# Kernel optimization log

Hardware: AMD Instinct MI355X
Metric: run time of the kernel (lower is better)

The kernel has to match this reference:

```python
import jax, jax.numpy as jnp
import numpy as np

NORMALIZE_EPS = 1e-5
INV_DELTA = 15.0
DIST_NORM_PREV = 0.5  # init value of _dist_norm_prev buffer (eval-mode constant)
SKIP_OFFSET = 2


def _l2_normalize(v, axis, eps=NORMALIZE_EPS):
    # matches torch F.normalize: v / max(||v||, eps)
    n = jnp.sqrt(jnp.sum(v * v, axis=axis, keepdims=True))
    return v / jnp.maximum(n, eps)


def setup_inputs() -> dict:
    key = jax.random.key(0)
    k1, k2 = jax.random.split(key)
    x = jax.random.normal(k1, (128, 197, 768), dtype=jnp.float32)
    emb = jnp.clip(jax.random.normal(k2, (4096, 768), dtype=jnp.float32), 0.0, None)
    emb = _l2_normalize(emb, axis=1)
    return {"x": x, "embedding": emb}


def reference(x, embedding):
    # drop CLS token -> [N, L, C] with L = H*W
    x = x[:, 1:, :]
    N, L, C = x.shape
    height = width = int(np.sqrt(L))
    # assign_words: L2-normalize tokens, cosine distance to codebook
    xn = _l2_normalize(x, axis=2)
    dist = -jnp.einsum("nlc,kc->nlk", xn, embedding)  # [N, L, K]
    inv_delta = INV_DELTA / DIST_NORM_PREV
    codes = jax.nn.softmax(-inv_delta * dist, axis=2)  # [N, L, K]
    # compute_bow: drop border tokens, mean-pool, L1-normalize
    grid = jnp.arange(height * width).reshape(height, width)
    keep = grid[SKIP_OFFSET:-SKIP_OFFSET, SKIP_OFFSET:-SKIP_OFFSET].reshape(-1)
    bow = jnp.mean(codes[:, keep, :], axis=1)  # [N, K]
    bow = bow / jnp.maximum(jnp.sum(jnp.abs(bow), axis=1, keepdims=True), NORMALIZE_EPS)
    return bow, codes
```

## Files before the change

kernel.cpp:

```cpp
#include <hip/hip_runtime.h>


typedef unsigned short ushort_t;
typedef short short8 __attribute__((ext_vector_type(8)));
typedef float float4_ __attribute__((ext_vector_type(4)));

#define M_ROWS 25088
#define N_COLS 4096
#define K_DIM  768
#define BM 128
#define BN 128
#define BK 32
#define K_STEPS (K_DIM / BK)

__device__ __forceinline__ unsigned short f2bf_rne(float f) {
  unsigned u = __float_as_uint(f);
  unsigned r = u + 0x7fffu + ((u >> 16) & 1u);
  return (unsigned short)(r >> 16);
}
__device__ __forceinline__ float bf2f(unsigned short h) {
  return __uint_as_float(((unsigned)h) << 16);
}

__device__ __forceinline__ void gload16(const void* g, void* l) {
  __builtin_amdgcn_global_load_lds(
      (__attribute__((address_space(1))) void*)g,
      (__attribute__((address_space(3))) void*)l, 16, 0, 0);
}

__global__ void split_emb_kernel(const float* __restrict__ emb,
                                 ushort_t* __restrict__ Bh,
                                 ushort_t* __restrict__ Bl) {
  int t = blockIdx.x * 256 + threadIdx.x;
  float f = emb[t];
  unsigned short h = f2bf_rne(f);
  Bh[t] = h;
  Bl[t] = f2bf_rne(f - bf2f(h));
}

__global__ void norm_split_x_kernel(const float* __restrict__ x,
                                    ushort_t* __restrict__ Ah,
                                    ushort_t* __restrict__ Al) {
  int m = blockIdx.x;
  int n = m / 196;
  int l = m - n * 196;
  size_t src = ((size_t)n * 197 + 1 + l) * 768;
  int t = threadIdx.x;

  float v0 = x[src + t];
  float v1 = x[src + t + 256];
  float v2 = x[src + t + 512];
  float s = v0 * v0 + v1 * v1 + v2 * v2;
  #pragma unroll
  for (int off = 32; off; off >>= 1) s += __shfl_xor(s, off, 64);
  __shared__ float ws4[4];
  if ((t & 63) == 0) ws4[t >> 6] = s;
  __syncthreads();
  s = ws4[0] + ws4[1] + ws4[2] + ws4[3];
  float scale = 1.0f / fmaxf(sqrtf(s), 1e-5f);

  size_t dst = (size_t)m * 768;
  float f[3] = {v0 * scale, v1 * scale, v2 * scale};
  int idx[3] = {t, t + 256, t + 512};
  #pragma unroll
  for (int i = 0; i < 3; i++) {
    unsigned short h = f2bf_rne(f[i]);
    Ah[dst + idx[i]] = h;
    Al[dst + idx[i]] = f2bf_rne(f[i] - bf2f(h));
  }
}

__global__ __launch_bounds__(256, 2)
void gemm_exp_kernel(const ushort_t* __restrict__ Ah, const ushort_t* __restrict__ Al,
                     const ushort_t* __restrict__ Bh, const ushort_t* __restrict__ Bl,
                     float* __restrict__ codes, float* __restrict__ rowsum) {
  __shared__ __attribute__((aligned(16))) ushort_t sAh[2][BM * BK];
  __shared__ __attribute__((aligned(16))) ushort_t sAl[2][BM * BK];
  __shared__ __attribute__((aligned(16))) ushort_t sBh[2][BM * BK];
  __shared__ __attribute__((aligned(16))) ushort_t sBl[2][BM * BK];
  __shared__ float rs[BM];

  const int t = threadIdx.x;
  const int w = t >> 6;
  const int lane = t & 63;
  const int row0 = blockIdx.x * BM;
  const int col0 = blockIdx.y * BN;

  if (t < BM) rs[t] = 0.f;

  float4_ acc[4][4];
  #pragma unroll
  for (int i = 0; i < 4; i++)
    #pragma unroll
    for (int j = 0; j < 4; j++) acc[i][j] = (float4_){0.f, 0.f, 0.f, 0.f};

  const int r0 = t >> 2;
  const int c0 = (((t & 3) ^ ((r0 >> 1) & 3))) * 8;
  const ushort_t* gA = Ah + (size_t)(row0 + r0) * K_DIM + c0;
  const ushort_t* gAl_ = Al + (size_t)(row0 + r0) * K_DIM + c0;
  const ushort_t* gB = Bh + (size_t)(col0 + r0) * K_DIM + c0;
  const ushort_t* gBl_ = Bl + (size_t)(col0 + r0) * K_DIM + c0;
  const int half = 64 * K_DIM;
  const int ldsw = w * 512;

  const int rl = (w >> 1) * 64;
  const int cl = (w & 1) * 64;
  const int lq = lane >> 4;
  const int li = lane & 15;
  const int fsw = (li >> 1) & 3;
  const int abase = (rl + li) * BK + (lq ^ fsw) * 8;
  const int bbase = (cl + li) * BK + (lq ^ fsw) * 8;

  auto issue = [&](int b, int kk) {
    gload16(gA + kk,           &sAh[b][ldsw]);
    gload16(gA + kk + half,    &sAh[b][2048 + ldsw]);
    gload16(gAl_ + kk,         &sAl[b][ldsw]);
    gload16(gAl_ + kk + half,  &sAl[b][2048 + ldsw]);
    gload16(gB + kk,           &sBh[b][ldsw]);
    gload16(gB + kk + half,    &sBh[b][2048 + ldsw]);
    gload16(gBl_ + kk,         &sBl[b][ldsw]);
    gload16(gBl_ + kk + half,  &sBl[b][2048 + ldsw]);
  };

  auto compute = [&](int b) {
    short8 ah[4], al[4], bh[4], bl[4];
    #pragma unroll
    for (int i = 0; i < 4; i++) {
      ah[i] = *(const short8*)(&sAh[b][abase + i * 16 * BK]);
      al[i] = *(const short8*)(&sAl[b][abase + i * 16 * BK]);
      bh[i] = *(const short8*)(&sBh[b][bbase + i * 16 * BK]);
      bl[i] = *(const short8*)(&sBl[b][bbase + i * 16 * BK]);
    }
    #pragma unroll
    for (int i = 0; i < 4; i++)
      #pragma unroll
      for (int j = 0; j < 4; j++) {
        acc[i][j] = __builtin_amdgcn_mfma_f32_16x16x32_bf16(ah[i], bh[j], acc[i][j], 0, 0, 0);
        acc[i][j] = __builtin_amdgcn_mfma_f32_16x16x32_bf16(ah[i], bl[j], acc[i][j], 0, 0, 0);
        acc[i][j] = __builtin_amdgcn_mfma_f32_16x16x32_bf16(al[i], bh[j], acc[i][j], 0, 0, 0);
      }
  };

  issue(0, 0);

  #pragma unroll 1
  for (int ks = 0; ks < K_STEPS - 2; ks += 2) {
    issue(1, (ks + 1) * BK);
    asm volatile("s_waitcnt vmcnt(8)" ::: "memory");
    __builtin_amdgcn_s_barrier();
    asm volatile("" ::: "memory");
    compute(0);
    asm volatile("" ::: "memory");
    __builtin_amdgcn_s_barrier();

    issue(0, (ks + 2) * BK);
    asm volatile("s_waitcnt vmcnt(8)" ::: "memory");
    __builtin_amdgcn_s_barrier();
    asm volatile("" ::: "memory");
    compute(1);
    asm volatile("" ::: "memory");
    __builtin_amdgcn_s_barrier();
  }

  issue(1, (K_STEPS - 1) * BK);
  asm volatile("s_waitcnt vmcnt(8)" ::: "memory");
  __builtin_amdgcn_s_barrier();
  asm volatile("" ::: "memory");
  compute(0);
  asm volatile("" ::: "memory");
  __builtin_amdgcn_s_barrier();

  asm volatile("s_waitcnt vmcnt(0)" ::: "memory");
  __builtin_amdgcn_s_barrier();
  asm volatile("" ::: "memory");
  compute(1);

  float rsum[4][4];
  #pragma unroll
  for (int i = 0; i < 4; i++)
    #pragma unroll
    for (int r = 0; r < 4; r++) rsum[i][r] = 0.f;

  #pragma unroll
  for (int i = 0; i < 4; i++)
    #pragma unroll
    for (int j = 0; j < 4; j++)
      #pragma unroll
      for (int r = 0; r < 4; r++) {
        float e = __expf(30.0f * acc[i][j][r]);
        size_t row = (size_t)(row0 + rl + i * 16 + lq * 4 + r);
        size_t col = (size_t)(col0 + cl + j * 16 + li);
        codes[row * N_COLS + col] = e;
        rsum[i][r] += e;
      }

  #pragma unroll
  for (int i = 0; i < 4; i++)
    #pragma unroll
    for (int r = 0; r < 4; r++) {
      float v = rsum[i][r];
      v += __shfl_xor(v, 1, 64);
      v += __shfl_xor(v, 2, 64);
      v += __shfl_xor(v, 4, 64);
      v += __shfl_xor(v, 8, 64);
      if (li == 0) atomicAdd(&rs[rl + i * 16 + lq * 4 + r], v);
    }
  __syncthreads();
  if (t < BM) atomicAdd(&rowsum[row0 + t], rs[t]);
}

__global__ __launch_bounds__(256)
void rescale_bow_kernel(float* __restrict__ codes,
                        const float* __restrict__ rowsum,
                        float* __restrict__ bow_un) {
  const int bid = blockIdx.x;
  const int n = bid >> 4;
  const int g = (bid >> 2) & 3;
  const int chunk = bid & 3;
  const int t = threadIdx.x;
  const int k4 = chunk * 256 + t;
  const int l0 = g * 49;

  __shared__ float inv[49];
  __shared__ float keep[49];
  if (t < 49) {
    int l = l0 + t;
    inv[t] = 1.0f / rowsum[n * 196 + l];
    int rr = l / 14;
    int cc = l - rr * 14;
    keep[t] = (rr >= 2 && rr <= 11 && cc >= 2 && cc <= 11) ? 0.01f : 0.0f;
  }
  __syncthreads();

  float4_* base = (float4_*)(codes + (size_t)n * 196 * N_COLS)
                  + (size_t)l0 * 1024 + k4;
  float4_ acc = {0.f, 0.f, 0.f, 0.f};
  #pragma unroll
  for (int c = 0; c < 7; c++) {
    float4_ v[7];
    #pragma unroll
    for (int u = 0; u < 7; u++) v[u] = base[(size_t)(c * 7 + u) * 1024];
    #pragma unroll
    for (int u = 0; u < 7; u++) {
      int l = c * 7 + u;
      float iv = inv[l];
      v[u].x *= iv; v[u].y *= iv; v[u].z *= iv; v[u].w *= iv;
      base[(size_t)l * 1024] = v[u];
      float kf = keep[l];
      acc.x += kf * v[u].x; acc.y += kf * v[u].y;
      acc.z += kf * v[u].z; acc.w += kf * v[u].w;
    }
  }

  float* dst = bow_un + (size_t)n * N_COLS + (size_t)k4 * 4;
  atomicAdd(dst + 0, acc.x);
  atomicAdd(dst + 1, acc.y);
  atomicAdd(dst + 2, acc.z);
  atomicAdd(dst + 3, acc.w);
}

__global__ __launch_bounds__(256)
void bow_norm_kernel(const float* __restrict__ bow_un,
                     float* __restrict__ bow_out) {
  const int n = blockIdx.x;
  const int t = threadIdx.x;
  const float4_* src = (const float4_*)(bow_un + (size_t)n * N_COLS);
  float4_ v[4];
  float s = 0.f;
  #pragma unroll
  for (int i = 0; i < 4; i++) {
    v[i] = src[t + i * 256];
    s += fabsf(v[i].x) + fabsf(v[i].y) + fabsf(v[i].z) + fabsf(v[i].w);
  }
  #pragma unroll
  for (int off = 32; off; off >>= 1) s += __shfl_xor(s, off, 64);
  __shared__ float ws4[4];
  if ((t & 63) == 0) ws4[t >> 6] = s;
  __syncthreads();
  float invn = 1.0f / fmaxf(ws4[0] + ws4[1] + ws4[2] + ws4[3], 1e-5f);
  float4_* dst = (float4_*)(bow_out + (size_t)n * N_COLS);
  #pragma unroll
  for (int i = 0; i < 4; i++) {
    float4_ o = v[i];
    o.x *= invn; o.y *= invn; o.z *= invn; o.w *= invn;
    dst[t + i * 256] = o;
  }
}

extern "C" void kernel_launch(void* const* d_in, const int* in_sizes, int n_in,
                              void* d_out, int out_size, void* d_ws, size_t ws_size,
                              hipStream_t stream) {
  const float* x = (const float*)d_in[0];
  const float* emb = (const float*)d_in[1];
  float* bow_out = (float*)d_out;
  float* codes = (float*)d_out + 524288;

  char* ws = (char*)d_ws;
  ushort_t* Ah = (ushort_t*)(ws + 0);
  ushort_t* Al = (ushort_t*)(ws + 38535168);
  ushort_t* Bh = (ushort_t*)(ws + 77070336);
  ushort_t* Bl = (ushort_t*)(ws + 83361792);
  float* rowsum = (float*)(ws + 89653248);
  float* bow_un = (float*)(ws + 89753600);

  hipMemsetAsync(rowsum, 0, 25088 * 4, stream);
  hipMemsetAsync(bow_un, 0, 524288 * 4, stream);

  split_emb_kernel<<<12288, 256, 0, stream>>>(emb, Bh, Bl);
  norm_split_x_kernel<<<25088, 256, 0, stream>>>(x, Ah, Al);

  dim3 ggrid(M_ROWS / BM, N_COLS / BN);
  gemm_exp_kernel<<<ggrid, 256, 0, stream>>>(Ah, Al, Bh, Bl, codes, rowsum);

  rescale_bow_kernel<<<2048, 256, 0, stream>>>(codes, rowsum, bow_un);
  bow_norm_kernel<<<128, 256, 0, stream>>>(bow_un, bow_out);
}
```

Baseline: 1.057 ms.

## Swap GEMM grid order and restructure rescale/bow reduction without atomics

Swaps the GEMM grid so consecutive blocks walk across codebook columns for the same row tile, which changes L2 reuse of the A rows versus the B panel. Each rescale block now processes all 196 tokens for its column chunk, so bow_un is written directly instead of via per-element atomics and its memset goes away. The L1 norm is accumulated per sample with one atomic per block, and the final normalize becomes a simple elementwise kernel. The rescale grid shrinks from 2048 to 512 blocks, which lowers parallelism for that memory-bound pass.

New measurement: 1.018 ms. -3.7%, faster.

```diff
diff --git a/kernel.cpp b/kernel.cpp
--- a/kernel.cpp
+++ b/kernel.cpp
@@ -83,8 +83,8 @@
   const int t = threadIdx.x;
   const int w = t >> 6;
   const int lane = t & 63;
-  const int row0 = blockIdx.x * BM;
-  const int col0 = blockIdx.y * BN;
+  const int row0 = blockIdx.y * BM;
+  const int col0 = blockIdx.x * BN;
 
   if (t < BM) rs[t] = 0.f;
 
@@ -212,37 +212,32 @@
 __global__ __launch_bounds__(256)
 void rescale_bow_kernel(float* __restrict__ codes,
                         const float* __restrict__ rowsum,
-                        float* __restrict__ bow_un) {
-  const int bid = blockIdx.x;
-  const int n = bid >> 4;
-  const int g = (bid >> 2) & 3;
-  const int chunk = bid & 3;
+                        float* __restrict__ bow_un,
+                        float* __restrict__ bow_l1) {
+  const int n = blockIdx.x >> 2;
   const int t = threadIdx.x;
-  const int k4 = chunk * 256 + t;
-  const int l0 = g * 49;
-
-  __shared__ float inv[49];
-  __shared__ float keep[49];
-  if (t < 49) {
-    int l = l0 + t;
-    inv[t] = 1.0f / rowsum[n * 196 + l];
-    int rr = l / 14;
-    int cc = l - rr * 14;
+  const int k4 = (blockIdx.x & 3) * 256 + t;
+
+  __shared__ float inv[196];
+  __shared__ float keep[196];
+  if (t < 196) {
+    inv[t] = 1.0f / rowsum[n * 196 + t];
+    int rr = t / 14;
+    int cc = t - rr * 14;
     keep[t] = (rr >= 2 && rr <= 11 && cc >= 2 && cc <= 11) ? 0.01f : 0.0f;
   }
   __syncthreads();
 
-  float4_* base = (float4_*)(codes + (size_t)n * 196 * N_COLS)
-                  + (size_t)l0 * 1024 + k4;
+  float4_* base = (float4_*)(codes + (size_t)n * 196 * N_COLS) + k4;
   float4_ acc = {0.f, 0.f, 0.f, 0.f};
-  #pragma unroll
-  for (int c = 0; c < 7; c++) {
-    float4_ v[7];
-    #pragma unroll
-    for (int u = 0; u < 7; u++) v[u] = base[(size_t)(c * 7 + u) * 1024];
-    #pragma unroll
-    for (int u = 0; u < 7; u++) {
-      int l = c * 7 + u;
+  #pragma unroll 1
+  for (int c = 0; c < 14; c++) {
+    float4_ v[14];
+    #pragma unroll
+    for (int u = 0; u < 14; u++) v[u] = base[(size_t)(c * 14 + u) * 1024];
+    #pragma unroll
+    for (int u = 0; u < 14; u++) {
+      int l = c * 14 + u;
       float iv = inv[l];
       v[u].x *= iv; v[u].y *= iv; v[u].z *= iv; v[u].w *= iv;
       base[(size_t)l * 1024] = v[u];
@@ -252,39 +247,23 @@
     }
   }
 
-  float* dst = bow_un + (size_t)n * N_COLS + (size_t)k4 * 4;
-  atomicAdd(dst + 0, acc.x);
-  atomicAdd(dst + 1, acc.y);
-  atomicAdd(dst + 2, acc.z);
-  atomicAdd(dst + 3, acc.w);
-}
-
-__global__ __launch_bounds__(256)
-void bow_norm_kernel(const float* __restrict__ bow_un,
-                     float* __restrict__ bow_out) {
-  const int n = blockIdx.x;
-  const int t = threadIdx.x;
-  const float4_* src = (const float4_*)(bow_un + (size_t)n * N_COLS);
-  float4_ v[4];
-  float s = 0.f;
-  #pragma unroll
-  for (int i = 0; i < 4; i++) {
-    v[i] = src[t + i * 256];
-    s += fabsf(v[i].x) + fabsf(v[i].y) + fabsf(v[i].z) + fabsf(v[i].w);
-  }
+  ((float4_*)(bow_un + (size_t)n * N_COLS))[k4] = acc;
+
+  float s = fabsf(acc.x) + fabsf(acc.y) + fabsf(acc.z) + fabsf(acc.w);
   #pragma unroll
   for (int off = 32; off; off >>= 1) s += __shfl_xor(s, off, 64);
-  __shared__ float ws4[4];
-  if ((t & 63) == 0) ws4[t >> 6] = s;
-  __syncthreads();
-  float invn = 1.0f / fmaxf(ws4[0] + ws4[1] + ws4[2] + ws4[3], 1e-5f);
-  float4_* dst = (float4_*)(bow_out + (size_t)n * N_COLS);
-  #pragma unroll
-  for (int i = 0; i < 4; i++) {
-    float4_ o = v[i];
-    o.x *= invn; o.y *= invn; o.z *= invn; o.w *= invn;
-    dst[t + i * 256] = o;
-  }
+  __shared__ float wsum[4];
+  if ((t & 63) == 0) wsum[t >> 6] = s;
+  __syncthreads();
+  if (t == 0) atomicAdd(&bow_l1[n], wsum[0] + wsum[1] + wsum[2] + wsum[3]);
+}
+
+__global__ void bow_norm_kernel(const float* __restrict__ bow_un,
+                                const float* __restrict__ bow_l1,
+                                float* __restrict__ bow_out) {
+  int t = blockIdx.x * 256 + threadIdx.x;
+  int n = t >> 12;
+  bow_out[t] = bow_un[t] / fmaxf(bow_l1[n], 1e-5f);
 }
 
 extern "C" void kernel_launch(void* const* d_in, const int* in_sizes, int n_in,
@@ -302,16 +281,17 @@
   ushort_t* Bl = (ushort_t*)(ws + 83361792);
   float* rowsum = (float*)(ws + 89653248);
   float* bow_un = (float*)(ws + 89753600);
+  float* bow_l1 = (float*)(ws + 91850752);
 
   hipMemsetAsync(rowsum, 0, 25088 * 4, stream);
-  hipMemsetAsync(bow_un, 0, 524288 * 4, stream);
+  hipMemsetAsync(bow_l1, 0, 128 * 4, stream);
 
   split_emb_kernel<<<12288, 256, 0, stream>>>(emb, Bh, Bl);
   norm_split_x_kernel<<<25088, 256, 0, stream>>>(x, Ah, Al);
 
-  dim3 ggrid(M_ROWS / BM, N_COLS / BN);
+  dim3 ggrid(N_COLS / BN, M_ROWS / BM);
   gemm_exp_kernel<<<ggrid, 256, 0, stream>>>(Ah, Al, Bh, Bl, codes, rowsum);
 
-  rescale_bow_kernel<<<2048, 256, 0, stream>>>(codes, rowsum, bow_un);
-  bow_norm_kernel<<<128, 256, 0, stream>>>(bow_un, bow_out);
-}
+  rescale_bow_kernel<<<512, 256, 0, stream>>>(codes, rowsum, bow_un, bow_l1);
+  bow_norm_kernel<<<2048, 256, 0, stream>>>(bow_un, bow_l1, bow_out);
+}
```
